# Kernel tuning notes

Measured on AMD Instinct MI355X. Metric: run time of the kernel, lower is better.

Reference implementation:

```python
import jax, jax.numpy as jnp
import numpy as np

K = 9          # neighbors
DIL = 1        # dilation
BN_EPS = 1e-5

def _bn(x, g, b, m, v):
    # inference batchnorm over channel (last) dim
    return (x - m) * (g * jax.lax.rsqrt(v + BN_EPS)) + b

def setup_inputs() -> dict:
    key = jax.random.key(0)
    ks = jax.random.split(key, 4)
    B, C, H, W = 8, 192, 56, 56
    Ch = 384
    s = 0.02
    return {
        'x': jax.random.normal(ks[0], (B, C, H, W), jnp.float32),
        'fc1_w': jax.random.normal(ks[1], (C, C), jnp.float32) * s,
        'fc1_b': jnp.zeros((C,), jnp.float32),
        'bn1_g': jnp.ones((C,), jnp.float32), 'bn1_b': jnp.zeros((C,), jnp.float32),
        'bn1_m': jnp.zeros((C,), jnp.float32), 'bn1_v': jnp.ones((C,), jnp.float32),
        'gc_w': jax.random.normal(ks[2], (Ch, 2 * C), jnp.float32) * s,
        'gc_b': jnp.zeros((Ch,), jnp.float32),
        'bn2_g': jnp.ones((Ch,), jnp.float32), 'bn2_b': jnp.zeros((Ch,), jnp.float32),
        'bn2_m': jnp.zeros((Ch,), jnp.float32), 'bn2_v': jnp.ones((Ch,), jnp.float32),
        'fc2_w': jax.random.normal(ks[3], (C, Ch), jnp.float32) * s,
        'fc2_b': jnp.zeros((C,), jnp.float32),
        'bn3_g': jnp.ones((C,), jnp.float32), 'bn3_b': jnp.zeros((C,), jnp.float32),
        'bn3_m': jnp.zeros((C,), jnp.float32), 'bn3_v': jnp.ones((C,), jnp.float32),
    }

def reference(x, fc1_w, fc1_b, bn1_g, bn1_b, bn1_m, bn1_v,
              gc_w, gc_b, bn2_g, bn2_b, bn2_m, bn2_v,
              fc2_w, fc2_b, bn3_g, bn3_b, bn3_m, bn3_v):
    B, C, H, W = x.shape
    N = H * W
    xf = x.reshape(B, C, N).transpose(0, 2, 1)          # (B, N, C) nodes
    shortcut = xf
    # fc1: 1x1 conv + BN
    h = _bn(jnp.einsum('bnc,oc->bno', xf, fc1_w) + fc1_b, bn1_g, bn1_b, bn1_m, bn1_v)
    # dynamic KNN on L2-normalized features (ViG dense_knn_matrix)
    hn = h / jnp.maximum(jnp.linalg.norm(h, axis=-1, keepdims=True), 1e-12)
    sim = jnp.einsum('bnc,bmc->bnm', hn, hn)            # (B, N, N) cosine sim
    _, idx = jax.lax.top_k(sim, K * DIL)                # nearest (incl. self)
    idx = idx[..., ::DIL]                               # dilated neighbors (B,N,K)
    # gather neighbor features
    x_j = jax.vmap(lambda hb, ib: hb[ib])(h, idx)       # (B, N, K, C)
    x_i = h[:, :, None, :]                              # (B, N, 1, C)
    feat = jnp.concatenate([jnp.broadcast_to(x_i, x_j.shape), x_j - x_i], axis=-1)
    # EdgeConv: conv then max over neighbors
    e = jnp.einsum('bnke,oe->bnko', feat, gc_w) + gc_b  # (B, N, K, Ch)
    m = jnp.max(e, axis=2)                              # (B, N, Ch)
    m = jax.nn.gelu(_bn(m, bn2_g, bn2_b, bn2_m, bn2_v), approximate=False)
    # fc2: 1x1 conv + BN, residual
    out = _bn(jnp.einsum('bnh,oh->bno', m, fc2_w) + fc2_b, bn3_g, bn3_b, bn3_m, bn3_v)
    out = out + shortcut
    return out.transpose(0, 2, 1).reshape(B, C, H, W)
```

## Files before the change

kernel.cpp:

```cpp
#include <hip/hip_runtime.h>

#define BDIM 256
#define NB 8
#define NC 192
#define NN 3136
#define NCH 384
#define NK 9
#define NROW (NB * NN)

typedef __attribute__((ext_vector_type(8))) short short8;
typedef __attribute__((ext_vector_type(4))) float f32x4;

__device__ __forceinline__ unsigned short f2bf(float f) {
  union { float f; unsigned u; } x{f};
  unsigned r = x.u + 0x7fff + ((x.u >> 16) & 1);
  return (unsigned short)(r >> 16);
}

__device__ __forceinline__ float bf2f(unsigned u16) {
  union { unsigned u; float f; } x{u16 << 16};
  return x.f;
}

__device__ __forceinline__ unsigned fsort(float f) {
  union { float f; unsigned u; } x{f};
  return x.u ^ ((unsigned)(((int)x.u) >> 31) | 0x80000000u);
}

__device__ __forceinline__ void stage_tile(const char* gbase, char* lbuf, int t) {
#pragma unroll
  for (int i = 0; i < 6; ++i) {
    int L = (i * 256 + t) * 16;
    int m = L / 384;
    int kb = L - m * 384;
    const char* g = gbase + m * 384 + (kb ^ ((m & 7) << 4));
    __builtin_amdgcn_global_load_lds(
        (const __attribute__((address_space(1))) unsigned int*)g,
        (__attribute__((address_space(3))) unsigned int*)(lbuf + L), 16, 0, 0);
  }
}

__device__ __forceinline__ void stage_tile32(const char* gbase, char* lbuf, int t) {
#pragma unroll
  for (int i = 0; i < 3; ++i) {
    int L = (i * 256 + t) * 16;
    int m = L / 384;
    int kb = L - m * 384;
    const char* g = gbase + m * 384 + (kb ^ ((m & 7) << 4));
    __builtin_amdgcn_global_load_lds(
        (const __attribute__((address_space(1))) unsigned int*)g,
        (__attribute__((address_space(3))) unsigned int*)(lbuf + L), 16, 0, 0);
  }
}

__global__ __launch_bounds__(BDIM) void k0_convw(
    const float* __restrict__ gw, const float* __restrict__ f1w,
    const float* __restrict__ f2w, unsigned short* __restrict__ gcwb,
    unsigned short* __restrict__ fc1b, unsigned short* __restrict__ fc2b) {
  int i = (blockIdx.x * BDIM + threadIdx.x) * 4;
  const float* src;
  unsigned short* dst;
  if (i < 147456) {
    int o = i / NC, k = i - o * NC;
    src = gw + (size_t)(o < NCH ? o : o - NCH) * (2 * NC) + (o < NCH ? 0 : NC) + k;
    dst = gcwb + i;
  } else if (i < 184320) {
    int j = i - 147456;
    src = f1w + j;
    dst = fc1b + j;
  } else {
    int j = i - 184320;
    int o = j / NCH, k = j - o * NCH;
    int oc = o >> 6, om = o & 63;
    int kh = k / 192, km = k - kh * 192;
    src = f2w + j;
    dst = fc2b + ((size_t)((oc * 2 + kh) * 64 + om)) * 192 + km;
  }
  float4 v = *(const float4*)src;
  uint2 u;
  u.x = (unsigned)f2bf(v.x) | ((unsigned)f2bf(v.y) << 16);
  u.y = (unsigned)f2bf(v.z) | ((unsigned)f2bf(v.w) << 16);
  *(uint2*)dst = u;
}

__global__ __launch_bounds__(384) void k0b_params(
    const float* __restrict__ f1b, const float* __restrict__ g1,
    const float* __restrict__ b1, const float* __restrict__ m1,
    const float* __restrict__ v1, const float* __restrict__ gcb,
    const float* __restrict__ g2, const float* __restrict__ b2,
    const float* __restrict__ m2, const float* __restrict__ v2,
    const float* __restrict__ f2b, const float* __restrict__ g3,
    const float* __restrict__ b3, const float* __restrict__ m3,
    const float* __restrict__ v3, float* __restrict__ sc1,
    float* __restrict__ sh1, float* __restrict__ sc2, float* __restrict__ sh2,
    float* __restrict__ sc3, float* __restrict__ sh3) {
  int c = threadIdx.x;
  if (c < NC) {
    float s1 = g1[c] * rsqrtf(v1[c] + 1e-5f);
    sc1[c] = s1;
    sh1[c] = (f1b[c] - m1[c]) * s1 + b1[c];
    float s3 = g3[c] * rsqrtf(v3[c] + 1e-5f);
    sc3[c] = s3;
    sh3[c] = (f2b[c] - m3[c]) * s3 + b3[c];
  }
  float s2 = g2[c] * rsqrtf(v2[c] + 1e-5f);
  sc2[c] = s2;
  sh2[c] = (gcb[c] - m2[c]) * s2 + b2[c];
}

__global__ __launch_bounds__(BDIM) void k1_mfma(
    const float* __restrict__ x, const unsigned short* __restrict__ fc1b,
    const float* __restrict__ sc1, const float* __restrict__ sh1,
    unsigned short* __restrict__ hnb, float* __restrict__ normo) {
  __shared__ __align__(16) char abuf[2][24576];
  int t = threadIdx.x;
  int b = blockIdx.x / 49, n0 = (blockIdx.x % 49) * 64;
  int lane = t & 63, w = t >> 6;
  int l15 = lane & 15, l4 = lane >> 4;
  int n = n0 + w * 16 + l15;
  short8 bfr[6];
  {
    const float* xcol = x + (size_t)b * NC * NN + n;
#pragma unroll
    for (int ks = 0; ks < 6; ++ks) {
      union { short8 s; unsigned u[4]; } pk;
#pragma unroll
      for (int j = 0; j < 4; ++j) {
        float v0 = xcol[(size_t)(ks * 32 + l4 * 8 + 2 * j) * NN];
        float v1 = xcol[(size_t)(ks * 32 + l4 * 8 + 2 * j + 1) * NN];
        pk.u[j] = (unsigned)f2bf(v0) | ((unsigned)f2bf(v1) << 16);
      }
      bfr[ks] = pk.s;
    }
  }
  f32x4 acc[3][4];
#pragma unroll
  for (int oc = 0; oc < 3; ++oc)
#pragma unroll
    for (int sub = 0; sub < 4; ++sub) acc[oc][sub] = {0.f, 0.f, 0.f, 0.f};

  const char* wB = (const char*)fc1b;
  stage_tile(wB, abuf[0], t);
  __syncthreads();
  for (int oc = 0; oc < 3; ++oc) {
    int cur = oc & 1;
    if (oc < 2) stage_tile(wB + (size_t)(oc + 1) * 24576, abuf[cur ^ 1], t);
#pragma unroll
    for (int sub = 0; sub < 4; ++sub) {
      int r_ = sub * 16 + l15;
      int rbase = r_ * 384, sw = (r_ & 7) << 4;
#pragma unroll
      for (int ks = 0; ks < 6; ++ks) {
        short8 af = *(const short8*)&abuf[cur][rbase + ((ks * 64 + l4 * 16) ^ sw)];
        acc[oc][sub] = __builtin_amdgcn_mfma_f32_16x16x32_bf16(af, bfr[ks],
                                                               acc[oc][sub], 0, 0, 0);
      }
    }
    __syncthreads();
  }
  float p = 0.f;
#pragma unroll
  for (int oc = 0; oc < 3; ++oc)
#pragma unroll
    for (int sub = 0; sub < 4; ++sub) {
      int c4 = oc * 64 + sub * 16 + l4 * 4;
      float s_[4], h_[4];
      *(float4*)s_ = *(const float4*)&sc1[c4];
      *(float4*)h_ = *(const float4*)&sh1[c4];
#pragma unroll
      for (int r = 0; r < 4; ++r) {
        float v = acc[oc][sub][r] * s_[r] + h_[r];
        acc[oc][sub][r] = v;
        p += v * v;
      }
    }
  p += __shfl_xor(p, 16);
  p += __shfl_xor(p, 32);
  float nr = fmaxf(sqrtf(p), 1e-12f);
  float iv = 1.f / nr;
  if (l4 == 0) normo[(size_t)b * NN + n] = nr;
#pragma unroll
  for (int oc = 0; oc < 3; ++oc)
#pragma unroll
    for (int sub = 0; sub < 4; ++sub) {
      uint2 u;
      u.x = (unsigned)f2bf(acc[oc][sub][0] * iv) |
            ((unsigned)f2bf(acc[oc][sub][1] * iv) << 16);
      u.y = (unsigned)f2bf(acc[oc][sub][2] * iv) |
            ((unsigned)f2bf(acc[oc][sub][3] * iv) << 16);
      *(uint2*)&hnb[(size_t)(b * NN + n) * NC + oc * 64 + sub * 16 + l4 * 4] = u;
    }
}

__global__ __launch_bounds__(BDIM) void k23_fused(
    const unsigned short* __restrict__ hnb, const float* __restrict__ norm,
    const unsigned short* __restrict__ gcwb, unsigned* __restrict__ candK,
    unsigned short* __restrict__ P, unsigned short* __restrict__ Q) {
  __shared__ __align__(16) char abuf[2][12288];
  int t = threadIdx.x;
  int bid = blockIdx.x;
  int b = bid & 7;
  int j = bid >> 3;
  int role3 = j % 3;
  int lane = t & 63, w = t >> 6;
  int l15 = lane & 15, l4 = lane >> 4;
  const unsigned short* hb = hnb + (size_t)b * NN * NC;

  if (role3 != 2) {
    int idx2a = (j / 3) * 2 + role3;
    int n0 = (idx2a >> 2) * 64;
    int seg = idx2a & 3;
    int mt0 = (98 * seg) / 4, mt1 = (98 * (seg + 1)) / 4;
    const char* hbB = (const char*)hb;

    short8 bfr[6];
    {
      const short8* brow =
          (const short8*)(hb + (size_t)(n0 + w * 16 + l15) * NC + l4 * 8);
#pragma unroll
      for (int ks = 0; ks < 6; ++ks) bfr[ks] = brow[ks * 4];
    }
    unsigned tk[NK];
#pragma unroll
    for (int r = 0; r < NK; ++r) tk[r] = 0u;

    stage_tile32(hbB + (size_t)mt0 * 12288, abuf[0], t);
    __syncthreads();
    int nt = mt1 - mt0;
    for (int ti = 0; ti < nt; ++ti) {
      int cur = ti & 1;
      if (ti + 1 < nt)
        stage_tile32(hbB + (size_t)(mt0 + ti + 1) * 12288, abuf[cur ^ 1], t);
      int mglob = (mt0 + ti) * 32;
#pragma unroll
      for (int sub = 0; sub < 2; ++sub) {
        int r_ = sub * 16 + l15;
        int rbase = r_ * 384, sw = (r_ & 7) << 4;
        short8 af[6];
#pragma unroll
        for (int ks = 0; ks < 6; ++ks)
          af[ks] = *(const short8*)&abuf[cur][rbase + ((ks * 64 + l4 * 16) ^ sw)];
        f32x4 acc = {0.f, 0.f, 0.f, 0.f};
#pragma unroll
        for (int ks = 0; ks < 6; ++ks)
          acc = __builtin_amdgcn_mfma_f32_16x16x32_bf16(af[ks], bfr[ks], acc, 0, 0, 0);
        int mknd = 4095 - (mglob + sub * 16 + l4 * 4);
#pragma unroll
        for (int r = 0; r < 4; ++r) {
          unsigned cur_k = (fsort(acc[r]) & 0xFFFFF000u) | (unsigned)(mknd - r);
#pragma unroll
          for (int q = 0; q < NK; ++q) {
            unsigned hi = tk[q] > cur_k ? tk[q] : cur_k;
            unsigned lo = tk[q] > cur_k ? cur_k : tk[q];
            tk[q] = hi;
            cur_k = lo;
          }
        }
      }
      __syncthreads();
    }
    unsigned* mkeys = (unsigned*)&abuf[0][0];
    int nl = w * 16 + l15;
#pragma unroll
    for (int r = 0; r < NK; ++r) mkeys[(nl * 4 + l4) * NK + r] = tk[r];
    __syncthreads();
    if (t < 64) {
      const unsigned* src = &mkeys[t * 4 * NK];
      unsigned best[NK];
#pragma unroll
      for (int r = 0; r < NK; ++r) best[r] = 0u;
      for (int s = 0; s < 36; ++s) {
        unsigned cur_k = src[s];
#pragma unroll
        for (int q = 0; q < NK; ++q) {
          unsigned hi = best[q] > cur_k ? best[q] : cur_k;
          unsigned lo = best[q] > cur_k ? cur_k : best[q];
          best[q] = hi;
          cur_k = lo;
        }
      }
      size_t row = (size_t)b * NN + n0 + t;
#pragma unroll
      for (int r = 0; r < NK; ++r)
        candK[(size_t)(seg * NK + r) * NROW + row] = best[r];
    }
  } else {
    int jj = j / 3;
    int n0 = (jj >> 1) * 64;
    int half = jj & 1;
    int n = n0 + w * 16 + l15;
    short8 bfr[6];
    {
      const short8* brow = (const short8*)(hb + (size_t)n * NC + l4 * 8);
#pragma unroll
      for (int ks = 0; ks < 6; ++ks) bfr[ks] = brow[ks * 4];
    }
    float nrm = norm[(size_t)b * NN + n];
    size_t orow = (size_t)b * NN + n;
    const char* wB = (const char*)gcwb;

    int ch0 = half * 12;
    stage_tile32(wB + (size_t)ch0 * 12288, abuf[0], t);
    __syncthreads();
    for (int ci = 0; ci < 12; ++ci) {
      int ch = ch0 + ci;
      int cur = ci & 1;
      if (ci < 11) stage_tile32(wB + (size_t)(ch + 1) * 12288, abuf[cur ^ 1], t);
#pragma unroll
      for (int sub = 0; sub < 2; ++sub) {
        int mrow = sub * 16 + l15;
        int rbase = mrow * 384, sw = (mrow & 7) << 4;
        f32x4 acc = {0.f, 0.f, 0.f, 0.f};
#pragma unroll
        for (int ks = 0; ks < 6; ++ks) {
          short8 af = *(const short8*)&abuf[cur][rbase + ((ks * 64 + l4 * 16) ^ sw)];
          acc = __builtin_amdgcn_mfma_f32_16x16x32_bf16(af, bfr[ks], acc, 0, 0, 0);
        }
        int o = ch * 32 + sub * 16 + l4 * 4;
        f32x4 st = acc * nrm;
        unsigned short* dst = (o < NCH) ? P : Q;
        int oo = (o < NCH) ? o : o - NCH;
        uint2 u;
        u.x = (unsigned)f2bf(st[0]) | ((unsigned)f2bf(st[1]) << 16);
        u.y = (unsigned)f2bf(st[2]) | ((unsigned)f2bf(st[3]) << 16);
        *(uint2*)&dst[orow * NCH + oo] = u;
      }
      __syncthreads();
    }
  }
}

__global__ __launch_bounds__(BDIM) void k2b_merge(const unsigned* __restrict__ candK,
                                                  int* __restrict__ idxo) {
  int row = blockIdx.x * BDIM + threadIdx.x;
  unsigned tk[NK];
#pragma unroll
  for (int r = 0; r < NK; ++r) tk[r] = 0u;
  for (int s = 0; s < 4 * NK; ++s) {
    unsigned cur = candK[(size_t)s * NROW + row];
#pragma unroll
    for (int j = 0; j < NK; ++j) {
      unsigned hi = tk[j] > cur ? tk[j] : cur;
      unsigned lo = tk[j] > cur ? cur : tk[j];
      tk[j] = hi;
      cur = lo;
    }
  }
#pragma unroll
  for (int r = 0; r < NK; ++r)
    idxo[(size_t)row * NK + r] = 4095 - (int)(tk[r] & 4095u);
}

__global__ __launch_bounds__(BDIM) void k4_gathermax(
    const unsigned short* __restrict__ P, const unsigned short* __restrict__ Q,
    const int* __restrict__ idx, const float* __restrict__ sc2,
    const float* __restrict__ sh2, unsigned short* __restrict__ mbh) {
  int t = threadIdx.x;
  int lane = t & 63, wv = t >> 6;
  int row = blockIdx.x * 4 + wv;
  int b = row / NN, n = row % NN;
  const int* ip = idx + (size_t)row * NK;
  int id[NK];
#pragma unroll
  for (int k = 0; k < NK; ++k) id[k] = ip[k];
  const unsigned short* Qb = Q + (size_t)b * NN * NCH;
  const unsigned short* Pr = P + (size_t)row * NCH;
  const unsigned short* Qr = Qb + (size_t)n * NCH;
#pragma unroll
  for (int j = 0; j < 3; ++j) {
    int o = j * 128 + lane * 2;
    float mx0 = -1e30f, mx1 = -1e30f;
#pragma unroll
    for (int k = 0; k < NK; ++k) {
      unsigned g = *(const unsigned*)&Qb[(size_t)id[k] * NCH + o];
      mx0 = fmaxf(mx0, bf2f(g & 0xffffu));
      mx1 = fmaxf(mx1, bf2f(g >> 16));
    }
    unsigned pv = *(const unsigned*)&Pr[o];
    unsigned qv = *(const unsigned*)&Qr[o];
    float2 ss = *(const float2*)&sc2[o];
    float2 hh = *(const float2*)&sh2[o];
    float e0 = bf2f(pv & 0xffffu) - bf2f(qv & 0xffffu) + mx0;
    float e1 = bf2f(pv >> 16) - bf2f(qv >> 16) + mx1;
    float y0 = e0 * ss.x + hh.x;
    float y1 = e1 * ss.y + hh.y;
    float ge0 = 0.5f * y0 * (1.f + erff(y0 * 0.70710678118654752f));
    float ge1 = 0.5f * y1 * (1.f + erff(y1 * 0.70710678118654752f));
    *(unsigned*)&mbh[(size_t)row * NCH + o] =
        (unsigned)f2bf(ge0) | ((unsigned)f2bf(ge1) << 16);
  }
}

__global__ __launch_bounds__(BDIM) void k5_mfma(
    const unsigned short* __restrict__ mbh, const unsigned short* __restrict__ fc2b,
    const float* __restrict__ sc3, const float* __restrict__ sh3,
    const float* __restrict__ x, float* __restrict__ out) {
  __shared__ __align__(16) char abuf[2][24576];
  int t = threadIdx.x;
  int bid = blockIdx.x;
  int b = bid / 147;
  int rem = bid % 147;
  int n0 = (rem / 3) * 64;
  int oc = rem % 3;
  int lane = t & 63, w = t >> 6;
  int l15 = lane & 15, l4 = lane >> 4;
  int n = n0 + w * 16 + l15;
  short8 bfr[12];
  {
    const short8* brow = (const short8*)(mbh + (size_t)(b * NN + n) * NCH + l4 * 8);
#pragma unroll
    for (int kh = 0; kh < 2; ++kh)
#pragma unroll
      for (int ks = 0; ks < 6; ++ks) bfr[kh * 6 + ks] = brow[kh * 24 + ks * 4];
  }
  f32x4 acc[4];
#pragma unroll
  for (int sub = 0; sub < 4; ++sub) acc[sub] = {0.f, 0.f, 0.f, 0.f};

  const char* wt = (const char*)fc2b + (size_t)oc * 2 * 24576;
  stage_tile(wt, abuf[0], t);
  __syncthreads();
  for (int kh = 0; kh < 2; ++kh) {
    if (kh == 0) stage_tile(wt + 24576, abuf[1], t);
#pragma unroll
    for (int sub = 0; sub < 4; ++sub) {
      int r_ = sub * 16 + l15;
      int rbase = r_ * 384, sw = (r_ & 7) << 4;
#pragma unroll
      for (int ks = 0; ks < 6; ++ks) {
        short8 af = *(const short8*)&abuf[kh][rbase + ((ks * 64 + l4 * 16) ^ sw)];
        acc[sub] = __builtin_amdgcn_mfma_f32_16x16x32_bf16(af, bfr[kh * 6 + ks],
                                                           acc[sub], 0, 0, 0);
      }
    }
    __syncthreads();
  }
  const float* xb_ = x + (size_t)b * NC * NN;
  float* ob = out + (size_t)b * NC * NN;
#pragma unroll
  for (int sub = 0; sub < 4; ++sub) {
    int c4 = oc * 64 + sub * 16 + l4 * 4;
    float s_[4], h_[4];
    *(float4*)s_ = *(const float4*)&sc3[c4];
    *(float4*)h_ = *(const float4*)&sh3[c4];
#pragma unroll
    for (int r = 0; r < 4; ++r) {
      size_t off = (size_t)(c4 + r) * NN + n;
      ob[off] = acc[sub][r] * s_[r] + h_[r] + xb_[off];
    }
  }
}

extern "C" void kernel_launch(void* const* d_in, const int* in_sizes, int n_in,
                              void* d_out, int out_size, void* d_ws, size_t ws_size,
                              hipStream_t stream) {
  const float* x = (const float*)d_in[0];
  const float* fc1_w = (const float*)d_in[1];
  const float* fc1_b = (const float*)d_in[2];
  const float* bn1_g = (const float*)d_in[3];
  const float* bn1_b = (const float*)d_in[4];
  const float* bn1_m = (const float*)d_in[5];
  const float* bn1_v = (const float*)d_in[6];
  const float* gc_w = (const float*)d_in[7];
  const float* gc_b = (const float*)d_in[8];
  const float* bn2_g = (const float*)d_in[9];
  const float* bn2_b = (const float*)d_in[10];
  const float* bn2_m = (const float*)d_in[11];
  const float* bn2_v = (const float*)d_in[12];
  const float* fc2_w = (const float*)d_in[13];
  const float* fc2_b = (const float*)d_in[14];
  const float* bn3_g = (const float*)d_in[15];
  const float* bn3_b = (const float*)d_in[16];
  const float* bn3_m = (const float*)d_in[17];
  const float* bn3_v = (const float*)d_in[18];

  size_t nrow = (size_t)NROW;
  size_t npq = (size_t)NB * NN * NCH;
  size_t nhb = (size_t)NB * NN * NC;
  unsigned short* Pb = (unsigned short*)d_ws;
  unsigned short* Qb = Pb + npq;
  unsigned short* mbh = Qb + npq;
  float* norm = (float*)(mbh + npq);
  int* idx = (int*)(norm + nrow);
  unsigned short* hnb = (unsigned short*)(idx + nrow * NK);
  unsigned short* gcwb = hnb + nhb;
  unsigned short* fc1b = gcwb + 768 * NC;
  unsigned short* fc2b = fc1b + NC * NC;
  unsigned* candK = (unsigned*)(fc2b + NC * NCH);
  float* sc1 = (float*)(candK + 4 * NK * nrow);
  float* sh1 = sc1 + NC;
  float* sc2 = sh1 + NC;
  float* sh2 = sc2 + NCH;
  float* sc3 = sh2 + NCH;
  float* sh3 = sc3 + NC;

  k0_convw<<<252, BDIM, 0, stream>>>(gc_w, fc1_w, fc2_w, gcwb, fc1b, fc2b);
  k0b_params<<<1, 384, 0, stream>>>(fc1_b, bn1_g, bn1_b, bn1_m, bn1_v, gc_b,
                                    bn2_g, bn2_b, bn2_m, bn2_v, fc2_b, bn3_g,
                                    bn3_b, bn3_m, bn3_v, sc1, sh1, sc2, sh2,
                                    sc3, sh3);
  k1_mfma<<<NB * 49, BDIM, 0, stream>>>(x, fc1b, sc1, sh1, hnb, norm);
  k23_fused<<<NB * 294, BDIM, 0, stream>>>(hnb, norm, gcwb, candK, Pb, Qb);
  k2b_merge<<<NROW / BDIM, BDIM, 0, stream>>>(candK, idx);
  k4_gathermax<<<(NB * NN) / 4, BDIM, 0, stream>>>(Pb, Qb, idx, sc2, sh2, mbh);
  k5_mfma<<<NB * 147, BDIM, 0, stream>>>(mbh, fc2b, sc3, sh3, x, (float*)d_out);
}
```

Before: 164.2 us.

## Widen fused KNN/EdgeConv kernel to 512 threads, splitting tile rows across waves

The fused similarity-topk / projection kernel now uses 512-thread blocks. Each of the two 16-row sub-tiles goes to its own group of four waves instead of one wave looping over both. The block role split changes from 2:1 to 4:1: each projection block now covers all 24 weight chunks, and the top-k partial lists are reduced in two stages through shared memory. The gather-max kernel also reorders block-to-row mapping so consecutive blocks interleave batches. The aim is more waves in flight to hide latency and fewer redundant B-fragment loads, at the cost of an extra reduction pass and heavier register use per block.

```diff
diff --git a/kernel.cpp b/kernel.cpp
--- a/kernel.cpp
+++ b/kernel.cpp
@@ -40,10 +40,18 @@
   }
 }
 
-__device__ __forceinline__ void stage_tile32(const char* gbase, char* lbuf, int t) {
-#pragma unroll
-  for (int i = 0; i < 3; ++i) {
-    int L = (i * 256 + t) * 16;
+__device__ __forceinline__ void stage32_512(const char* gbase, char* lbuf, int t) {
+  {
+    int L = t * 16;
+    int m = L / 384;
+    int kb = L - m * 384;
+    const char* g = gbase + m * 384 + (kb ^ ((m & 7) << 4));
+    __builtin_amdgcn_global_load_lds(
+        (const __attribute__((address_space(1))) unsigned int*)g,
+        (__attribute__((address_space(3))) unsigned int*)(lbuf + L), 16, 0, 0);
+  }
+  if (t < 256) {
+    int L = (512 + t) * 16;
     int m = L / 384;
     int kb = L - m * 384;
     const char* g = gbase + m * 384 + (kb ^ ((m & 7) << 4));
@@ -192,7 +200,7 @@
     }
 }
 
-__global__ __launch_bounds__(BDIM) void k23_fused(
+__global__ __launch_bounds__(512) void k23_fused(
     const unsigned short* __restrict__ hnb, const float* __restrict__ norm,
     const unsigned short* __restrict__ gcwb, unsigned* __restrict__ candK,
     unsigned short* __restrict__ P, unsigned short* __restrict__ Q) {
@@ -201,13 +209,13 @@
   int bid = blockIdx.x;
   int b = bid & 7;
   int j = bid >> 3;
-  int role3 = j % 3;
   int lane = t & 63, w = t >> 6;
   int l15 = lane & 15, l4 = lane >> 4;
+  int wg = w & 3, sub = w >> 2;
   const unsigned short* hb = hnb + (size_t)b * NN * NC;
 
-  if (role3 != 2) {
-    int idx2a = (j / 3) * 2 + role3;
+  if (j % 5 != 4) {
+    int idx2a = (j / 5) * 4 + (j % 5);
     int n0 = (idx2a >> 2) * 64;
     int seg = idx2a & 3;
     int mt0 = (98 * seg) / 4, mt1 = (98 * (seg + 1)) / 4;
@@ -216,7 +224,7 @@
     short8 bfr[6];
     {
       const short8* brow =
-          (const short8*)(hb + (size_t)(n0 + w * 16 + l15) * NC + l4 * 8);
+          (const short8*)(hb + (size_t)(n0 + wg * 16 + l15) * NC + l4 * 8);
 #pragma unroll
       for (int ks = 0; ks < 6; ++ks) bfr[ks] = brow[ks * 4];
     }
@@ -224,53 +232,52 @@
 #pragma unroll
     for (int r = 0; r < NK; ++r) tk[r] = 0u;
 
-    stage_tile32(hbB + (size_t)mt0 * 12288, abuf[0], t);
+    int r_ = sub * 16 + l15;
+    int rbase = r_ * 384, sw = (r_ & 7) << 4;
+    stage32_512(hbB + (size_t)mt0 * 12288, abuf[0], t);
     __syncthreads();
     int nt = mt1 - mt0;
     for (int ti = 0; ti < nt; ++ti) {
       int cur = ti & 1;
       if (ti + 1 < nt)
-        stage_tile32(hbB + (size_t)(mt0 + ti + 1) * 12288, abuf[cur ^ 1], t);
-      int mglob = (mt0 + ti) * 32;
-#pragma unroll
-      for (int sub = 0; sub < 2; ++sub) {
-        int r_ = sub * 16 + l15;
-        int rbase = r_ * 384, sw = (r_ & 7) << 4;
-        short8 af[6];
-#pragma unroll
-        for (int ks = 0; ks < 6; ++ks)
-          af[ks] = *(const short8*)&abuf[cur][rbase + ((ks * 64 + l4 * 16) ^ sw)];
-        f32x4 acc = {0.f, 0.f, 0.f, 0.f};
-#pragma unroll
-        for (int ks = 0; ks < 6; ++ks)
-          acc = __builtin_amdgcn_mfma_f32_16x16x32_bf16(af[ks], bfr[ks], acc, 0, 0, 0);
-        int mknd = 4095 - (mglob + sub * 16 + l4 * 4);
-#pragma unroll
-        for (int r = 0; r < 4; ++r) {
-          unsigned cur_k = (fsort(acc[r]) & 0xFFFFF000u) | (unsigned)(mknd - r);
-#pragma unroll
-          for (int q = 0; q < NK; ++q) {
-            unsigned hi = tk[q] > cur_k ? tk[q] : cur_k;
-            unsigned lo = tk[q] > cur_k ? cur_k : tk[q];
-            tk[q] = hi;
-            cur_k = lo;
-          }
+        stage32_512(hbB + (size_t)(mt0 + ti + 1) * 12288, abuf[cur ^ 1], t);
+      short8 af[6];
+#pragma unroll
+      for (int ks = 0; ks < 6; ++ks)
+        af[ks] = *(const short8*)&abuf[cur][rbase + ((ks * 64 + l4 * 16) ^ sw)];
+      f32x4 acc = {0.f, 0.f, 0.f, 0.f};
+#pragma unroll
+      for (int ks = 0; ks < 6; ++ks)
+        acc = __builtin_amdgcn_mfma_f32_16x16x32_bf16(af[ks], bfr[ks], acc, 0, 0, 0);
+      int mknd = 4095 - ((mt0 + ti) * 32 + sub * 16 + l4 * 4);
+#pragma unroll
+      for (int r = 0; r < 4; ++r) {
+        unsigned cur_k = (fsort(acc[r]) & 0xFFFFF000u) | (unsigned)(mknd - r);
+#pragma unroll
+        for (int q = 0; q < NK; ++q) {
+          unsigned hi = tk[q] > cur_k ? tk[q] : cur_k;
+          unsigned lo = tk[q] > cur_k ? cur_k : tk[q];
+          tk[q] = hi;
+          cur_k = lo;
         }
       }
       __syncthreads();
     }
     unsigned* mkeys = (unsigned*)&abuf[0][0];
-    int nl = w * 16 + l15;
-#pragma unroll
-    for (int r = 0; r < NK; ++r) mkeys[(nl * 4 + l4) * NK + r] = tk[r];
+    int rw = wg * 16 + l15;
+#pragma unroll
+    for (int r = 0; r < NK; ++r) mkeys[(rw * 8 + sub * 4 + l4) * NK + r] = tk[r];
     __syncthreads();
-    if (t < 64) {
-      const unsigned* src = &mkeys[t * 4 * NK];
+    if (t < 256) {
+      int row = t >> 2, g = t & 3;
+      unsigned* a = &mkeys[(row * 8 + g) * NK];
+      const unsigned* c = &mkeys[(row * 8 + g + 4) * NK];
       unsigned best[NK];
 #pragma unroll
       for (int r = 0; r < NK; ++r) best[r] = 0u;
-      for (int s = 0; s < 36; ++s) {
-        unsigned cur_k = src[s];
+#pragma unroll
+      for (int s = 0; s < 2 * NK; ++s) {
+        unsigned cur_k = s < NK ? a[s] : c[s - NK];
 #pragma unroll
         for (int q = 0; q < NK; ++q) {
           unsigned hi = best[q] > cur_k ? best[q] : cur_k;
@@ -279,16 +286,34 @@
           cur_k = lo;
         }
       }
+#pragma unroll
+      for (int r = 0; r < NK; ++r) a[r] = best[r];
+    }
+    __syncthreads();
+    if (t < 64) {
+      const unsigned* src = &mkeys[(t * 8) * NK];
+      unsigned best[NK];
+#pragma unroll
+      for (int r = 0; r < NK; ++r) best[r] = 0u;
+      for (int s = 0; s < 36; ++s) {
+        unsigned cur_k = src[s];
+#pragma unroll
+        for (int q = 0; q < NK; ++q) {
+          unsigned hi = best[q] > cur_k ? best[q] : cur_k;
+          unsigned lo = best[q] > cur_k ? cur_k : best[q];
+          best[q] = hi;
+          cur_k = lo;
+        }
+      }
       size_t row = (size_t)b * NN + n0 + t;
 #pragma unroll
       for (int r = 0; r < NK; ++r)
         candK[(size_t)(seg * NK + r) * NROW + row] = best[r];
     }
   } else {
-    int jj = j / 3;
-    int n0 = (jj >> 1) * 64;
-    int half = jj & 1;
-    int n = n0 + w * 16 + l15;
+    int jj = j / 5;
+    int n0 = jj * 64;
+    int n = n0 + wg * 16 + l15;
     short8 bfr[6];
     {
       const short8* brow = (const short8*)(hb + (size_t)n * NC + l4 * 8);
@@ -298,33 +323,28 @@
     float nrm = norm[(size_t)b * NN + n];
     size_t orow = (size_t)b * NN + n;
     const char* wB = (const char*)gcwb;
-
-    int ch0 = half * 12;
-    stage_tile32(wB + (size_t)ch0 * 12288, abuf[0], t);
+    int mrow = sub * 16 + l15;
+    int rbase = mrow * 384, sw = (mrow & 7) << 4;
+
+    stage32_512(wB, abuf[0], t);
     __syncthreads();
-    for (int ci = 0; ci < 12; ++ci) {
-      int ch = ch0 + ci;
-      int cur = ci & 1;
-      if (ci < 11) stage_tile32(wB + (size_t)(ch + 1) * 12288, abuf[cur ^ 1], t);
-#pragma unroll
-      for (int sub = 0; sub < 2; ++sub) {
-        int mrow = sub * 16 + l15;
-        int rbase = mrow * 384, sw = (mrow & 7) << 4;
-        f32x4 acc = {0.f, 0.f, 0.f, 0.f};
-#pragma unroll
-        for (int ks = 0; ks < 6; ++ks) {
-          short8 af = *(const short8*)&abuf[cur][rbase + ((ks * 64 + l4 * 16) ^ sw)];
-          acc = __builtin_amdgcn_mfma_f32_16x16x32_bf16(af, bfr[ks], acc, 0, 0, 0);
-        }
-        int o = ch * 32 + sub * 16 + l4 * 4;
-        f32x4 st = acc * nrm;
-        unsigned short* dst = (o < NCH) ? P : Q;
-        int oo = (o < NCH) ? o : o - NCH;
-        uint2 u;
-        u.x = (unsigned)f2bf(st[0]) | ((unsigned)f2bf(st[1]) << 16);
-        u.y = (unsigned)f2bf(st[2]) | ((unsigned)f2bf(st[3]) << 16);
-        *(uint2*)&dst[orow * NCH + oo] = u;
-      }
+    for (int ch = 0; ch < 24; ++ch) {
+      int cur = ch & 1;
+      if (ch < 23) stage32_512(wB + (size_t)(ch + 1) * 12288, abuf[cur ^ 1], t);
+      f32x4 acc = {0.f, 0.f, 0.f, 0.f};
+#pragma unroll
+      for (int ks = 0; ks < 6; ++ks) {
+        short8 af = *(const short8*)&abuf[cur][rbase + ((ks * 64 + l4 * 16) ^ sw)];
+        acc = __builtin_amdgcn_mfma_f32_16x16x32_bf16(af, bfr[ks], acc, 0, 0, 0);
+      }
+      int o = ch * 32 + sub * 16 + l4 * 4;
+      f32x4 st = acc * nrm;
+      unsigned short* dst = (o < NCH) ? P : Q;
+      int oo = (o < NCH) ? o : o - NCH;
+      uint2 u;
+      u.x = (unsigned)f2bf(st[0]) | ((unsigned)f2bf(st[1]) << 16);
+      u.y = (unsigned)f2bf(st[2]) | ((unsigned)f2bf(st[3]) << 16);
+      *(uint2*)&dst[orow * NCH + oo] = u;
       __syncthreads();
     }
   }
@@ -357,14 +377,15 @@
     const float* __restrict__ sh2, unsigned short* __restrict__ mbh) {
   int t = threadIdx.x;
   int lane = t & 63, wv = t >> 6;
-  int row = blockIdx.x * 4 + wv;
-  int b = row / NN, n = row % NN;
-  const int* ip = idx + (size_t)row * NK;
+  int b = blockIdx.x & 7;
+  int n = (int)(blockIdx.x >> 3) * 4 + wv;
+  size_t row = (size_t)b * NN + n;
+  const int* ip = idx + row * NK;
   int id[NK];
 #pragma unroll
   for (int k = 0; k < NK; ++k) id[k] = ip[k];
   const unsigned short* Qb = Q + (size_t)b * NN * NCH;
-  const unsigned short* Pr = P + (size_t)row * NCH;
+  const unsigned short* Pr = P + row * NCH;
   const unsigned short* Qr = Qb + (size_t)n * NCH;
 #pragma unroll
   for (int j = 0; j < 3; ++j) {
@@ -386,7 +407,7 @@
     float y1 = e1 * ss.y + hh.y;
     float ge0 = 0.5f * y0 * (1.f + erff(y0 * 0.70710678118654752f));
     float ge1 = 0.5f * y1 * (1.f + erff(y1 * 0.70710678118654752f));
-    *(unsigned*)&mbh[(size_t)row * NCH + o] =
+    *(unsigned*)&mbh[row * NCH + o] =
         (unsigned)f2bf(ge0) | ((unsigned)f2bf(ge1) << 16);
   }
 }
@@ -500,7 +521,7 @@
                                     bn3_b, bn3_m, bn3_v, sc1, sh1, sc2, sh2,
                                     sc3, sh3);
   k1_mfma<<<NB * 49, BDIM, 0, stream>>>(x, fc1b, sc1, sh1, hnb, norm);
-  k23_fused<<<NB * 294, BDIM, 0, stream>>>(hnb, norm, gcwb, candK, Pb, Qb);
+  k23_fused<<<NB * 245, 512, 0, stream>>>(hnb, norm, gcwb, candK, Pb, Qb);
   k2b_merge<<<NROW / BDIM, BDIM, 0, stream>>>(candK, idx);
   k4_gathermax<<<(NB * NN) / 4, BDIM, 0, stream>>>(Pb, Qb, idx, sc2, sh2, mbh);
   k5_mfma<<<NB * 147, BDIM, 0, stream>>>(mbh, fc2b, sc3, sh3, x, (float*)d_out);
```

Result: faster. 158.3 us (-3.6%).
